# Kernel optimization log

Measured on AMD Instinct MI355X. Metric: run time of the kernel, lower is better.

Reference implementation:

```python
import jax, jax.numpy as jnp
import numpy as np
from jax import lax

B_, NF, H, W = 2, 8, 32, 32
DIM = 384            # mamba_feat_dim = pT*pH*pW*hid_dim = 2*2*2*48
D_INNER = 192        # expand=0.5 -> int(0.5*384)
D_STATE = 16
D_CONV = 4
DT_RANK = 24         # ceil(DIM/16)
HIDDEN = 1536        # mlp_ratio=4
L = NF * H * W


def _ln(x, w, b):
    m = x.mean(-1, keepdims=True)
    v = ((x - m) ** 2).mean(-1, keepdims=True)
    return (x - m) * lax.rsqrt(v + 1e-5) * w + b


def _mamba(xn, in_proj_w, conv_w, conv_b, xproj_w, dt_w, dt_b, A_log, Dp, out_proj_w):
    # xn: [b, L, DIM]
    b = xn.shape[0]
    xz = jnp.einsum('bld,ed->ble', xn, in_proj_w)            # [b,L,2*di]
    xp, z = xz[..., :D_INNER], xz[..., D_INNER:]
    # causal depthwise conv along L (mamba_ssm pads left d_conv-1)
    xc = lax.conv_general_dilated(xp.swapaxes(1, 2), conv_w[:, None, :], (1,),
                                  [(D_CONV - 1, 0)],
                                  dimension_numbers=('NCH', 'OIH', 'NCH'),
                                  feature_group_count=D_INNER) + conv_b[None, :, None]
    xc = jax.nn.silu(xc).swapaxes(1, 2)                      # [b,L,di]
    dbl = jnp.einsum('bld,ed->ble', xc, xproj_w)             # [b,L,dt_rank+2*ds]
    dt = jax.nn.softplus(jnp.einsum('blr,dr->bld', dbl[..., :DT_RANK], dt_w) + dt_b)
    Bm = dbl[..., DT_RANK:DT_RANK + D_STATE]
    Cm = dbl[..., DT_RANK + D_STATE:]
    A = -jnp.exp(A_log)                                      # [di,ds]

    def step(h, inp):
        dt_t, B_t, C_t, x_t = inp                            # [b,di],[b,ds],[b,ds],[b,di]
        dA = jnp.exp(dt_t[..., None] * A)                    # [b,di,ds]
        h = dA * h + dt_t[..., None] * B_t[:, None, :] * x_t[..., None]
        return h, jnp.einsum('bds,bs->bd', h, C_t)

    h0 = jnp.zeros((b, D_INNER, D_STATE), xn.dtype)
    _, ys = lax.scan(step, h0, (dt.swapaxes(0, 1), Bm.swapaxes(0, 1),
                                Cm.swapaxes(0, 1), xc.swapaxes(0, 1)))
    y = ys.swapaxes(0, 1) + Dp * xc
    y = y * jax.nn.silu(z)
    return jnp.einsum('ble,de->bld', y, out_proj_w)


def _ssa(seqs, ssa_w):
    # sequence shuffle attention: grouped 1x1 conv over per-sequence pooled features
    pooled = jnp.stack([s.mean(1) for s in seqs], 1)          # [b,3,c]
    w = jnp.einsum('bsd,dts->btd', pooled, ssa_w)             # per-channel 3x3 mix
    aw = jax.nn.softmax(w, axis=1)                            # softmax over sequences
    st = jnp.stack(seqs, 0)                                   # [3,b,L,c]
    return jnp.einsum('btd,tbld->bld', aw, st)


def _mlp(x, fc1_w, fc1_b, dw_w, dw_b, fc2_w, fc2_b):
    b = x.shape[0]
    h1 = jnp.einsum('bld,ed->ble', x, fc1_w) + fc1_b          # [b,L,HIDDEN]
    hv = h1.swapaxes(1, 2).reshape(b, HIDDEN, NF, H, W)
    hv = lax.conv_general_dilated(hv, dw_w, (1, 1, 1), [(1, 1)] * 3,
                                  dimension_numbers=('NCDHW', 'OIDHW', 'NCDHW'),
                                  feature_group_count=HIDDEN) + dw_b[None, :, None, None, None]
    h1 = hv.reshape(b, HIDDEN, L).swapaxes(1, 2)
    h1 = jax.nn.gelu(h1, approximate=False)
    return jnp.einsum('ble,de->bld', h1, fc2_w) + fc2_b


def _forward(x, freq_x, ln1_w, ln1_b, in_proj_w, conv_w, conv_b, xproj_w, dt_w, dt_b,
             A_log, Dp, out_proj_w, ssa_w, ln2_w, ln2_b, fc1_w, fc1_b, dw_w, dw_b,
             fc2_w, fc2_b, hilbert_curve):
    b = x.shape[0]
    xc = x.transpose(0, 2, 1, 3, 4).reshape(b, DIM, L)        # [b,c,L]
    x_flat = xc[:, :, hilbert_curve].swapaxes(1, 2)           # hilbert gather -> [b,L,c]
    fc = freq_x.transpose(0, 2, 1, 3, 4).reshape(b, DIM, L)
    f_flat = fc[:, :, hilbert_curve].swapaxes(1, 2)
    normed = _ln(x_flat, ln1_w, ln1_b)
    mparams = (in_proj_w, conv_w, conv_b, xproj_w, dt_w, dt_b, A_log, Dp, out_proj_w)
    m_fwd = _mamba(normed, *mparams)
    m_rev = jnp.flip(_mamba(jnp.flip(normed, 1), *mparams), 1)
    mo = _ssa([m_fwd, m_rev, f_flat], ssa_w)
    xm = x_flat + mo
    xm = xm + _mlp(_ln(xm, ln2_w, ln2_b), fc1_w, fc1_b, dw_w, dw_b, fc2_w, fc2_b)
    outm = xm.swapaxes(1, 2)                                  # [b,c,L]
    inv = jnp.argsort(hilbert_curve)                          # inverse permutation (scatter)
    uns = outm[:, :, inv]
    return uns.reshape(b, DIM, NF, H, W).transpose(0, 2, 1, 3, 4)


def setup_inputs() -> dict:
    key = jax.random.key(0)
    ks = jax.random.split(key, 12)
    def n(i, shape, s=0.02):
        return jax.random.normal(ks[i], shape, jnp.float32) * s
    perm = jnp.asarray(np.random.default_rng(0).permutation(L), jnp.int32)
    return {
        'x': jax.random.normal(ks[0], (B_, NF, DIM, H, W), jnp.float32),
        'freq_x': jax.random.normal(ks[1], (B_, NF, DIM, H, W), jnp.float32),
        'hilbert_curve': perm,
        'ln1_w': jnp.ones((DIM,), jnp.float32), 'ln1_b': jnp.zeros((DIM,), jnp.float32),
        'in_proj_w': n(2, (2 * D_INNER, DIM)),
        'conv_w': n(3, (D_INNER, D_CONV), 0.1), 'conv_b': jnp.zeros((D_INNER,), jnp.float32),
        'xproj_w': n(4, (DT_RANK + 2 * D_STATE, D_INNER)),
        'dt_w': n(5, (D_INNER, DT_RANK), 0.1),
        'dt_b': jnp.full((D_INNER,), -4.6, jnp.float32),
        'A_log': jnp.log(jnp.tile(jnp.arange(1, D_STATE + 1, dtype=jnp.float32)[None, :], (D_INNER, 1))),
        'Dp': jnp.ones((D_INNER,), jnp.float32),
        'out_proj_w': n(6, (DIM, D_INNER)),
        'ssa_w': n(7, (DIM, 3, 3)),
        'ln2_w': jnp.ones((DIM,), jnp.float32), 'ln2_b': jnp.zeros((DIM,), jnp.float32),
        'fc1_w': n(8, (HIDDEN, DIM)), 'fc1_b': jnp.zeros((HIDDEN,), jnp.float32),
        'dw_w': n(9, (HIDDEN, 1, 3, 3, 3), 0.05), 'dw_b': jnp.zeros((HIDDEN,), jnp.float32),
        'fc2_w': n(10, (DIM, HIDDEN)), 'fc2_b': jnp.zeros((DIM,), jnp.float32),
    }


def reference(x, freq_x, hilbert_curve, ln1_w, ln1_b, in_proj_w, conv_w, conv_b,
              xproj_w, dt_w, dt_b, A_log, Dp, out_proj_w, ssa_w, ln2_w, ln2_b,
              fc1_w, fc1_b, dw_w, dw_b, fc2_w, fc2_b):
    return _forward(x, freq_x, ln1_w, ln1_b, in_proj_w, conv_w, conv_b, xproj_w,
                    dt_w, dt_b, A_log, Dp, out_proj_w, ssa_w, ln2_w, ln2_b,
                    fc1_w, fc1_b, dw_w, dw_b, fc2_w, fc2_b, hilbert_curve)
```

## Files before the change

### kernel.cpp

```cpp
#include <hip/hip_runtime.h>
#include <cmath>

#define B_N 2
#define NFR 8
#define HH 32
#define WW 32
#define LSEQ 8192
#define DIMD 384
#define DI 192
#define DST 16
#define DRK 24
#define HID 1536
#define MR (B_N*LSEQ)

#define NCH 256
#define CL  (LSEQ/NCH)
#define PSL 128

typedef __attribute__((ext_vector_type(8))) short  bf16x8;
typedef __attribute__((ext_vector_type(4))) float  f32x4;
typedef __attribute__((ext_vector_type(8))) unsigned short u16x8;

constexpr size_t SZ_BLD = (size_t)MR * DIMD;
constexpr size_t SZ_BLI = (size_t)MR * DI;
constexpr size_t SZ_DBL = (size_t)MR * 56;

constexpr size_t OFF_XFLAT = 0;
constexpr size_t OFF_FFLAT = OFF_XFLAT + SZ_BLD;
constexpr size_t OFF_XZ    = OFF_FFLAT + SZ_BLD;
constexpr size_t OFF_XCF   = OFF_XZ + SZ_BLD;
constexpr size_t OFF_XCR   = OFF_XCF + SZ_BLI;
constexpr size_t OFF_H1    = 0;
constexpr size_t OFF_R2    = OFF_XCR + SZ_BLI;
constexpr size_t OFF_DBLF  = OFF_R2;
constexpr size_t OFF_DBLR  = OFF_DBLF + SZ_DBL;
constexpr size_t OFF_DTF   = OFF_DBLR + SZ_DBL;
constexpr size_t OFF_DTR   = OFF_DTF + SZ_BLI;
constexpr size_t OFF_GF    = OFF_DTR + SZ_BLI;
constexpr size_t OFF_GR    = OFF_GF + SZ_BLI;
constexpr size_t OFF_MF    = OFF_GR + SZ_BLI;
constexpr size_t OFF_MR_   = OFF_MF + SZ_BLD;
constexpr size_t OFF_H2    = OFF_R2;
constexpr size_t OFF_NORM  = OFF_MR_ + SZ_BLD;
constexpr size_t OFF_XM    = OFF_NORM + SZ_BLD;
constexpr size_t OFF_PART  = OFF_XM + SZ_BLD;
constexpr size_t OFF_AW    = OFF_PART + (size_t)6*PSL*384;
constexpr size_t OFF_INV   = OFF_AW + 2*3*384;
constexpr size_t SZ_CH   = (size_t)2*B_N*NCH*DI*16;
constexpr size_t OFF_CA  = OFF_NORM;
constexpr size_t OFF_CB  = OFF_CA + SZ_CH;
constexpr size_t OFF_CHS = OFF_CB + SZ_CH;
static_assert(OFF_CHS + SZ_CH <= OFF_PART, "scan summaries overflow");

__device__ __forceinline__ float siluf(float x){ return x / (1.f + expf(-x)); }
__device__ __forceinline__ float softplusf(float x){ return x > 20.f ? x : log1pf(expf(x)); }
__device__ __forceinline__ float geluf(float x){ return 0.5f * x * (1.f + erff(x * 0.70710678118f)); }
__device__ __forceinline__ unsigned short f2bf(float f){
    union { float f; unsigned int u; } v; v.f = f;
    unsigned int u = v.u + 0x7fffu + ((v.u >> 16) & 1u);
    return (unsigned short)(u >> 16);
}

#if __has_builtin(__builtin_amdgcn_global_load_lds)
#define HAVE_GLL 1
__device__ __forceinline__ void gload16(const void* g, void* l){
    __builtin_amdgcn_global_load_lds((const __attribute__((address_space(1))) void*)g,
                                     (__attribute__((address_space(3))) void*)l, 16, 0, 0);
}
#else
#define HAVE_GLL 0
#endif

__global__ __launch_bounds__(256)
void k_inv(const int* __restrict__ hc, int* __restrict__ inv)
{
    int l = blockIdx.x*256 + threadIdx.x;
    inv[hc[l]] = l;
}

__global__ __launch_bounds__(256)
void k_gather_ln(const float* __restrict__ x, const float* __restrict__ fx,
                 const int* __restrict__ inv, const float* __restrict__ lw,
                 const float* __restrict__ lb, float* __restrict__ x_flat,
                 float* __restrict__ f_flat, unsigned short* __restrict__ normed)
{
    __shared__ float tile[DIMD*33];
    int hw0 = blockIdx.x * 32;
    int nf  = blockIdx.y;
    int b   = blockIdx.z;
    int t   = threadIdx.x;
    int hwi = t & 31, dr = t >> 5;
    int w = t >> 6, lane = t & 63;
    const float* xb = x  + ((size_t)(b*NFR+nf)*DIMD)*1024 + hw0;
    const float* fb = fx + ((size_t)(b*NFR+nf)*DIMD)*1024 + hw0;

    for (int d0 = 0; d0 < DIMD; d0 += 8){
        int d = d0 + dr;
        tile[d*33 + hwi] = xb[(size_t)d*1024 + hwi];
    }
    __syncthreads();
    #pragma unroll
    for (int i = 0; i < 8; ++i){
        int r = w*8 + i;
        int l = inv[nf*1024 + hw0 + r];
        size_t rowo = (size_t)(b*LSEQ + l)*DIMD;
        float v[6]; float s = 0.f, s2 = 0.f;
        #pragma unroll
        for (int c = 0; c < 6; ++c){
            float a = tile[(c*64 + lane)*33 + r];
            v[c] = a; s += a; s2 += a*a;
        }
        #pragma unroll
        for (int o = 1; o < 64; o <<= 1){ s += __shfl_xor(s, o); s2 += __shfl_xor(s2, o); }
        float mean = s * (1.f/DIMD);
        float var  = s2 * (1.f/DIMD) - mean*mean;
        float rs = rsqrtf(var + 1e-5f);
        #pragma unroll
        for (int c = 0; c < 6; ++c){
            int d = c*64 + lane;
            x_flat[rowo + d] = v[c];
            normed[rowo + d] = f2bf((v[c]-mean)*rs*lw[d] + lb[d]);
        }
    }
    __syncthreads();
    for (int d0 = 0; d0 < DIMD; d0 += 8){
        int d = d0 + dr;
        tile[d*33 + hwi] = fb[(size_t)d*1024 + hwi];
    }
    __syncthreads();
    #pragma unroll
    for (int i = 0; i < 8; ++i){
        int r = w*8 + i;
        int l = inv[nf*1024 + hw0 + r];
        size_t rowo = (size_t)(b*LSEQ + l)*DIMD;
        #pragma unroll
        for (int c = 0; c < 6; ++c)
            f_flat[rowo + c*64 + lane] = tile[(c*64 + lane)*33 + r];
    }
}

__global__ __launch_bounds__(256)
void k_scatter(const float* __restrict__ outm, const int* __restrict__ inv,
               float* __restrict__ outp)
{
    __shared__ float tile[DIMD*33];
    int hw0 = blockIdx.x * 32;
    int nf  = blockIdx.y;
    int b   = blockIdx.z;
    int t   = threadIdx.x;
    int hwi = t & 31, dr = t >> 5;
    int w = t >> 6, lane = t & 63;
    #pragma unroll
    for (int i = 0; i < 8; ++i){
        int r = w*8 + i;
        int l = inv[nf*1024 + hw0 + r];
        const float* row = outm + (size_t)(b*LSEQ + l)*DIMD;
        #pragma unroll
        for (int c = 0; c < 6; ++c)
            tile[(c*64 + lane)*33 + r] = row[c*64 + lane];
    }
    __syncthreads();
    float* ob = outp + ((size_t)(b*NFR+nf)*DIMD)*1024 + hw0;
    for (int d0 = 0; d0 < DIMD; d0 += 8){
        int d = d0 + dr;
        ob[(size_t)d*1024 + hwi] = tile[d*33 + hwi];
    }
}

__global__ __launch_bounds__(128)
void k_ln(const float* __restrict__ in, const float* __restrict__ lw,
          const float* __restrict__ lb, unsigned short* __restrict__ out)
{
    size_t row = blockIdx.x;
    int t = threadIdx.x;
    float v[3]; float s = 0.f, s2 = 0.f;
    #pragma unroll
    for (int i = 0; i < 3; ++i){
        int d = t + i*128;
        float a = in[row*DIMD + d];
        v[i] = a; s += a; s2 += a*a;
    }
    #pragma unroll
    for (int o = 32; o > 0; o >>= 1){ s += __shfl_down(s, o); s2 += __shfl_down(s2, o); }
    __shared__ float sh[4];
    if ((t & 63) == 0){ sh[(t>>6)*2] = s; sh[(t>>6)*2+1] = s2; }
    __syncthreads();
    float S = sh[0] + sh[2], S2 = sh[1] + sh[3];
    float mean = S * (1.f/DIMD);
    float var  = S2 * (1.f/DIMD) - mean*mean;
    float r = rsqrtf(var + 1e-5f);
    #pragma unroll
    for (int i = 0; i < 3; ++i){
        int d = t + i*128;
        out[row*DIMD + d] = f2bf((v[i]-mean)*r*lw[d] + lb[d]);
    }
}

template<int EPI>
__global__ __launch_bounds__(256, 2)
void k_bgemm(const unsigned short* __restrict__ A, const float* __restrict__ Wf,
             const float* __restrict__ bias, const float* __restrict__ add,
             float* __restrict__ C, int N, int K)
{
    __shared__ unsigned short As[128*32];
    __shared__ unsigned short Bs[128*48];
    int tid  = threadIdx.x;
    int wid  = tid >> 6, lane = tid & 63;
    int row0 = blockIdx.x * 128, col0 = blockIdx.y * 128;
    int wr = wid >> 1, wc = wid & 1;
    int lr = lane & 15, lg = lane >> 4;

    f32x4 acc[4][4];
    #pragma unroll
    for (int m = 0; m < 4; ++m)
        #pragma unroll
        for (int n = 0; n < 4; ++n) acc[m][n] = (f32x4){0.f,0.f,0.f,0.f};

    int sA0 = wid*2048 + lane*16;
    int rA0 = sA0 >> 6, kA0 = (sA0 & 63) >> 1;
    int sA1 = sA0 + 1024;
    int rA1 = sA1 >> 6, kA1 = (sA1 & 63) >> 1;
    const unsigned short* Ag0 = A + (size_t)(row0 + rA0)*K + kA0;
    const unsigned short* Ag1 = A + (size_t)(row0 + rA1)*K + kA1;
    int bn = tid >> 1, bkp = (tid & 1) * 16;
    const float* Wg = Wf + (size_t)(col0 + bn)*K + bkp;

    const unsigned short* Ab = &As[(wr*64 + lr)*32 + lg*8];
    const unsigned short* Bb = &Bs[(wc*64 + lr)*48 + lg*8];
    unsigned short* Bw = &Bs[bn*48 + bkp];

    for (int k0 = 0; k0 < K; k0 += 32){
        if (k0) __syncthreads();
#if HAVE_GLL
        gload16(Ag0, (char*)As + wid*2048);
        gload16(Ag1, (char*)As + wid*2048 + 1024);
#else
        *(u16x8*)((char*)As + sA0) = *(const u16x8*)Ag0;
        *(u16x8*)((char*)As + sA1) = *(const u16x8*)Ag1;
#endif
        Ag0 += 32; Ag1 += 32;
        {
            float4 f0 = *(const float4*)(Wg+0);
            float4 f1 = *(const float4*)(Wg+4);
            float4 f2 = *(const float4*)(Wg+8);
            float4 f3 = *(const float4*)(Wg+12);
            Wg += 32;
            u16x8 p0, p1;
            p0[0]=f2bf(f0.x); p0[1]=f2bf(f0.y); p0[2]=f2bf(f0.z); p0[3]=f2bf(f0.w);
            p0[4]=f2bf(f1.x); p0[5]=f2bf(f1.y); p0[6]=f2bf(f1.z); p0[7]=f2bf(f1.w);
            p1[0]=f2bf(f2.x); p1[1]=f2bf(f2.y); p1[2]=f2bf(f2.z); p1[3]=f2bf(f2.w);
            p1[4]=f2bf(f3.x); p1[5]=f2bf(f3.y); p1[6]=f2bf(f3.z); p1[7]=f2bf(f3.w);
            *(u16x8*)(Bw)     = p0;
            *(u16x8*)(Bw + 8) = p1;
        }
        __syncthreads();
        bf16x8 af[4], bfr[4];
        #pragma unroll
        for (int m = 0; m < 4; ++m) af[m]  = *(const bf16x8*)(Ab + m*512);
        #pragma unroll
        for (int n = 0; n < 4; ++n) bfr[n] = *(const bf16x8*)(Bb + n*768);
        #pragma unroll
        for (int m = 0; m < 4; ++m)
            #pragma unroll
            for (int n = 0; n < 4; ++n)
                acc[m][n] = __builtin_amdgcn_mfma_f32_16x16x32_bf16(af[m], bfr[n], acc[m][n], 0, 0, 0);
    }

    #pragma unroll
    for (int m = 0; m < 4; ++m){
        #pragma unroll
        for (int r = 0; r < 4; ++r){
            int row = row0 + wr*64 + m*16 + lg*4 + r;
            #pragma unroll
            for (int n = 0; n < 4; ++n){
                int col = col0 + wc*64 + n*16 + lr;
                float v = acc[m][n][r];
                if (EPI >= 1) v += bias[col];
                if (EPI == 2) v += add[(size_t)row*N + col];
                C[(size_t)row*N + col] = v;
            }
        }
    }
}

__global__ __launch_bounds__(256)
void k_conv(const float* __restrict__ xz, const float* __restrict__ cw,
            const float* __restrict__ cb, float* __restrict__ xcf, float* __restrict__ xcr)
{
    const int TL = 64;
    int b = blockIdx.y;
    int l0 = blockIdx.x * TL;
    __shared__ float sx[TL+6][DI];
    for (int idx = threadIdx.x; idx < (TL+6)*DI; idx += 256){
        int r = idx / DI, c = idx % DI;
        int l = l0 + r - 3;
        float v = 0.f;
        if (l >= 0 && l < LSEQ) v = xz[((size_t)b*LSEQ + l)*DIMD + c];
        sx[r][c] = v;
    }
    __syncthreads();
    for (int idx = threadIdx.x; idx < TL*DI; idx += 256){
        int r = idx / DI, c = idx % DI;
        float w0 = cw[c*4+0], w1 = cw[c*4+1], w2 = cw[c*4+2], w3 = cw[c*4+3];
        float bi = cb[c];
        size_t orow = ((size_t)b*LSEQ + l0 + r)*DI + c;
        float af = bi + sx[r][c]*w0 + sx[r+1][c]*w1 + sx[r+2][c]*w2 + sx[r+3][c]*w3;
        xcf[orow] = siluf(af);
        float ar = bi + sx[r+3][c]*w3 + sx[r+4][c]*w2 + sx[r+5][c]*w1 + sx[r+6][c]*w0;
        xcr[orow] = siluf(ar);
    }
}

__global__ __launch_bounds__(256)
void k_dbl(const float* __restrict__ xc_f, const float* __restrict__ xc_r,
           const float* __restrict__ xpw,
           float* __restrict__ dbl_f, float* __restrict__ dbl_r)
{
    const float* xc  = blockIdx.y ? xc_r  : xc_f;
    float*       dbl = blockIdx.y ? dbl_r : dbl_f;
    __shared__ float sw[56*196];
    for (int i = threadIdx.x; i < 56*DI; i += 256){
        int n = i / DI, k = i % DI;
        sw[n*196 + k] = xpw[i];
    }
    __syncthreads();
    int lane = threadIdx.x & 63;
    int wid  = threadIdx.x >> 6;
    if (lane >= 56) return;
    const float* wrow = &sw[lane*196];
    #pragma unroll
    for (int g = 0; g < 2; ++g){
        int row0 = blockIdx.x*64 + g*32 + wid*8;
        const float* xr = xc + (size_t)row0*DI;
        float acc[8];
        #pragma unroll
        for (int r = 0; r < 8; ++r) acc[r] = 0.f;
        for (int k = 0; k < DI; k += 4){
            float4 w4 = *(const float4*)&wrow[k];
            #pragma unroll
            for (int r = 0; r < 8; ++r){
                float4 x4 = *(const float4*)&xr[(size_t)r*DI + k];
                acc[r] += x4.x*w4.x + x4.y*w4.y + x4.z*w4.z + x4.w*w4.w;
            }
        }
        #pragma unroll
        for (int r = 0; r < 8; ++r)
            dbl[(size_t)(row0 + r)*56 + lane] = acc[r];
    }
}

__global__ __launch_bounds__(192)
void k_dt(const float* __restrict__ dbl_f, const float* __restrict__ dbl_r,
          const float* __restrict__ dtw, const float* __restrict__ dtb,
          float* __restrict__ dt_f, float* __restrict__ dt_r)
{
    const float* dbl = blockIdx.y ? dbl_r : dbl_f;
    float*       dt  = blockIdx.y ? dt_r  : dt_f;
    int row0 = blockIdx.x * 8;
    int d = threadIdx.x;
    __shared__ float sd[8][24];
    {
        int lr = threadIdx.x / 24, lc = threadIdx.x % 24;
        sd[lr][lc] = dbl[(size_t)(row0 + lr)*56 + lc];
    }
    __syncthreads();
    float wreg[24];
    #pragma unroll
    for (int r = 0; r < DRK; ++r) wreg[r] = dtw[d*DRK + r];
    float bias = dtb[d];
    #pragma unroll
    for (int rr = 0; rr < 8; ++rr){
        float acc = bias;
        #pragma unroll
        for (int r = 0; r < DRK; ++r) acc += sd[rr][r] * wreg[r];
        dt[(size_t)(row0 + rr)*DI + d] = softplusf(acc);
    }
}

__global__ __launch_bounds__(384)
void k_scan_p1(const float* __restrict__ dt_f, const float* __restrict__ dt_r,
               const float* __restrict__ dbl_f, const float* __restrict__ dbl_r,
               const float* __restrict__ xc_f, const float* __restrict__ xc_r,
               const float* __restrict__ A_log,
               float* __restrict__ CA, float* __restrict__ CB)
{
    int ch = blockIdx.x, b = blockIdx.y, dir = blockIdx.z;
    const float* dt  = dir ? dt_r  : dt_f;
    const float* dbl = dir ? dbl_r : dbl_f;
    const float* xc  = dir ? xc_r  : xc_f;
    int t = threadIdx.x;
    int d = t >> 1, sh = (t & 1) * 8;
    float A2[8];
    #pragma unroll
    for (int s = 0; s < 8; ++s) A2[s] = -expf(A_log[d*DST + sh + s]) * 1.44269504f;
    float hB[8];
    #pragma unroll
    for (int s = 0; s < 8; ++s) hB[s] = 0.f;
    float sumdt = 0.f;
    __shared__ float sB[16][16];
    for (int t0 = 0; t0 < CL/16; ++t0){
        __syncthreads();
        if (t < 256){
            int j = t >> 4, c = t & 15;
            int lidx = ch*CL + t0*16 + j;
            int lld = dir ? (LSEQ-1-lidx) : lidx;
            sB[j][c] = dbl[((size_t)b*LSEQ + lld)*56 + 24 + c];
        }
        __syncthreads();
        for (int j = 0; j < 16; ++j){
            int lidx = ch*CL + t0*16 + j;
            int lld = dir ? (LSEQ-1-lidx) : lidx;
            size_t rowbl = (size_t)b*LSEQ + lld;
            float dtv = dt[rowbl*DI + d];
            float xv  = xc[rowbl*DI + d];
            float c0 = dtv * xv;
            sumdt += dtv;
            #pragma unroll
            for (int s = 0; s < 8; ++s){
                float da = exp2f(dtv * A2[s]);
                hB[s] = da*hB[s] + c0*sB[j][sh + s];
            }
        }
    }
    size_t o = (((size_t)(dir*B_N + b)*NCH + ch)*DI + d)*16 + sh;
    #pragma unroll
    for (int s = 0; s < 8; ++s){
        CA[o + s] = exp2f(sumdt * A2[s]);
        CB[o + s] = hB[s];
    }
}

__global__ __launch_bounds__(256)
void k_scan_p2(const float* __restrict__ CA, const float* __restrict__ CB,
               float* __restrict__ CH)
{
    int b = blockIdx.y, dir = blockIdx.z;
    int t = blockIdx.x*256 + threadIdx.x;
    size_t base = ((size_t)(dir*B_N + b)*NCH)*(DI*16) + t;
    float h = 0.f;
    for (int c = 0; c < NCH; ++c){
        size_t o = base + (size_t)c*(DI*16);
        CH[o] = h;
        h = CA[o]*h + CB[o];
    }
}

__global__ __launch_bounds__(384)
void k_scan_p3(const float* __restrict__ dt_f, const float* __restrict__ dt_r,
               const float* __restrict__ dbl_f, const float* __restrict__ dbl_r,
               const float* __restrict__ xc_f, const float* __restrict__ xc_r,
               const float* __restrict__ xz, const float* __restrict__ A_log,
               const float* __restrict__ Dp, const float* __restrict__ CH,
               unsigned short* __restrict__ g_f, unsigned short* __restrict__ g_r)
{
    int ch = blockIdx.x, b = blockIdx.y, dir = blockIdx.z;
    const float* dt  = dir ? dt_r  : dt_f;
    const float* dbl = dir ? dbl_r : dbl_f;
    const float* xc  = dir ? xc_r  : xc_f;
    unsigned short* g = dir ? g_r : g_f;
    int t = threadIdx.x;
    int d = t >> 1, sh = (t & 1) * 8;
    float A2[8];
    #pragma unroll
    for (int s = 0; s < 8; ++s) A2[s] = -expf(A_log[d*DST + sh + s]) * 1.44269504f;
    float Dpd = Dp[d];
    float h[8];
    size_t so = (((size_t)(dir*B_N + b)*NCH + ch)*DI + d)*16 + sh;
    #pragma unroll
    for (int s = 0; s < 8; ++s) h[s] = CH[so + s];
    __shared__ float sBC[16][32];
    for (int t0 = 0; t0 < CL/16; ++t0){
        __syncthreads();
        for (int idx = t; idx < 512; idx += 384){
            int j = idx >> 5, c = idx & 31;
            int lidx = ch*CL + t0*16 + j;
            int lld = dir ? (LSEQ-1-lidx) : lidx;
            sBC[j][c] = dbl[((size_t)b*LSEQ + lld)*56 + 24 + c];
        }
        __syncthreads();
        for (int j = 0; j < 16; ++j){
            int lidx = ch*CL + t0*16 + j;
            int lld = dir ? (LSEQ-1-lidx) : lidx;
            size_t rowbl = (size_t)b*LSEQ + lld;
            float dtv = dt[rowbl*DI + d];
            float xv  = xc[rowbl*DI + d];
            float zv  = xz[rowbl*DIMD + DI + d];
            float c0 = dtv * xv;
            float y = 0.f;
            #pragma unroll
            for (int s = 0; s < 8; ++s){
                float da = exp2f(dtv * A2[s]);
                h[s] = da*h[s] + c0*sBC[j][sh + s];
                y += h[s]*sBC[j][16 + sh + s];
            }
            y += __shfl_xor(y, 1);
            if ((t & 1) == 0)
                g[rowbl*DI + d] = f2bf((y + Dpd*xv) * siluf(zv));
        }
    }
}

__global__ __launch_bounds__(384)
void k_pool(const float* __restrict__ m_f, const float* __restrict__ m_r,
            const float* __restrict__ f_flat, float* __restrict__ partial)
{
    int bt = blockIdx.x;
    int sl = blockIdx.y;
    int b = bt / 3, t = bt % 3;
    const float* src = (t == 0) ? m_f : (t == 1) ? m_r : f_flat;
    src += (size_t)b*LSEQ*DIMD + (size_t)sl*(LSEQ/PSL)*DIMD;
    int d = threadIdx.x;
    float sum = 0.f;
    #pragma unroll 8
    for (int l = 0; l < LSEQ/PSL; ++l) sum += src[(size_t)l*DIMD + d];
    partial[((size_t)bt*PSL + sl)*DIMD + d] = sum;
}

__global__ __launch_bounds__(384)
void k_ssa(const float* __restrict__ partial, const float* __restrict__ ssaw,
           float* __restrict__ aw)
{
    int b = blockIdx.x;
    int d = threadIdx.x;
    float pooled[3];
    #pragma unroll
    for (int t = 0; t < 3; ++t){
        float sum = 0.f;
        for (int sl = 0; sl < PSL; ++sl) sum += partial[((size_t)(b*3+t)*PSL + sl)*DIMD + d];
        pooled[t] = sum * (1.f/LSEQ);
    }
    float wv[3];
    #pragma unroll
    for (int t = 0; t < 3; ++t)
        wv[t] = pooled[0]*ssaw[d*9 + t*3 + 0] + pooled[1]*ssaw[d*9 + t*3 + 1] + pooled[2]*ssaw[d*9 + t*3 + 2];
    float mx = fmaxf(wv[0], fmaxf(wv[1], wv[2]));
    float e0 = expf(wv[0]-mx), e1 = expf(wv[1]-mx), e2 = expf(wv[2]-mx);
    float inv_ = 1.f / (e0+e1+e2);
    aw[(size_t)(b*3+0)*DIMD + d] = e0*inv_;
    aw[(size_t)(b*3+1)*DIMD + d] = e1*inv_;
    aw[(size_t)(b*3+2)*DIMD + d] = e2*inv_;
}

__global__ __launch_bounds__(256)
void k_xm(const float* __restrict__ x_flat, const float* __restrict__ m_f,
          const float* __restrict__ m_r, const float* __restrict__ f_flat,
          const float* __restrict__ aw, float* __restrict__ xm)
{
    size_t idx = (size_t)blockIdx.x*256 + threadIdx.x;
    int d = (int)(idx % DIMD);
    size_t row = idx / DIMD;
    int b = (int)(row >> 13);
    float a0 = aw[(size_t)(b*3+0)*DIMD + d];
    float a1 = aw[(size_t)(b*3+1)*DIMD + d];
    float a2 = aw[(size_t)(b*3+2)*DIMD + d];
    xm[idx] = x_flat[idx] + a0*m_f[idx] + a1*m_r[idx] + a2*f_flat[idx];
}

__global__ __launch_bounds__(256)
void k_dwconv(const float* __restrict__ h1, const float* __restrict__ dww,
              const float* __restrict__ dwb, unsigned short* __restrict__ h2)
{
    int c = blockIdx.x*256 + threadIdx.x;
    int hy = blockIdx.y;
    int h = hy >> 1, w0 = (hy & 1) * 16;
    int bnf = blockIdx.z; int b = bnf >> 3, nf = bnf & 7;
    float wt[27];
    #pragma unroll
    for (int i = 0; i < 27; ++i) wt[i] = dww[(size_t)c*27 + i];
    float bias = dwb[c];
    bool nfok[3], hok[3];
    #pragma unroll
    for (int dd = 0; dd < 3; ++dd){
        nfok[dd] = (nf+dd-1) >= 0 && (nf+dd-1) < NFR;
        hok[dd]  = (h+dd-1)  >= 0 && (h+dd-1)  < HH;
    }
    const float* base = h1 + (size_t)b*LSEQ*HID + c;
    float win[3][3][3];
    #pragma unroll
    for (int dn = 0; dn < 3; ++dn)
        #pragma unroll
        for (int dh = 0; dh < 3; ++dh){
            bool ok = nfok[dn] && hok[dh];
            size_t rb = ((size_t)(nf+dn-1)*1024 + (size_t)(h+dh-1)*32);
            win[dn][dh][0] = (ok && w0 > 0) ? base[(rb + w0-1)*HID] : 0.f;
            win[dn][dh][1] = ok ? base[(rb + w0  )*HID] : 0.f;
            win[dn][dh][2] = ok ? base[(rb + w0+1)*HID] : 0.f;
        }
    unsigned short* orow = h2 + ((size_t)b*LSEQ + nf*1024 + h*32)*HID + c;
    #pragma unroll
    for (int xw = 0; xw < 16; ++xw){
        float acc = bias;
        #pragma unroll
        for (int dn = 0; dn < 3; ++dn)
            #pragma unroll
            for (int dh = 0; dh < 3; ++dh)
                #pragma unroll
                for (int dw = 0; dw < 3; ++dw)
                    acc += win[dn][dh][dw] * wt[dn*9 + dh*3 + dw];
        orow[(size_t)(w0 + xw)*HID] = f2bf(geluf(acc));
        int wn = w0 + xw + 2;
        #pragma unroll
        for (int dn = 0; dn < 3; ++dn)
            #pragma unroll
            for (int dh = 0; dh < 3; ++dh){
                win[dn][dh][0] = win[dn][dh][1];
                win[dn][dh][1] = win[dn][dh][2];
                bool ok = (wn < WW) && nfok[dn] && hok[dh];
                size_t rb = ((size_t)(nf+dn-1)*1024 + (size_t)(h+dh-1)*32);
                win[dn][dh][2] = ok ? base[(rb + wn)*HID] : 0.f;
            }
    }
}

extern "C" void kernel_launch(void* const* d_in, const int* in_sizes, int n_in,
                              void* d_out, int out_size, void* d_ws, size_t ws_size,
                              hipStream_t stream)
{
    const float* x     = (const float*)d_in[0];
    const float* fx    = (const float*)d_in[1];
    const int*   hc    = (const int*)  d_in[2];
    const float* ln1w  = (const float*)d_in[3];
    const float* ln1b  = (const float*)d_in[4];
    const float* inpw  = (const float*)d_in[5];
    const float* convw = (const float*)d_in[6];
    const float* convb = (const float*)d_in[7];
    const float* xpw   = (const float*)d_in[8];
    const float* dtw   = (const float*)d_in[9];
    const float* dtb   = (const float*)d_in[10];
    const float* alog  = (const float*)d_in[11];
    const float* dp    = (const float*)d_in[12];
    const float* outpw = (const float*)d_in[13];
    const float* ssaw  = (const float*)d_in[14];
    const float* ln2w  = (const float*)d_in[15];
    const float* ln2b  = (const float*)d_in[16];
    const float* fc1w  = (const float*)d_in[17];
    const float* fc1b  = (const float*)d_in[18];
    const float* dww   = (const float*)d_in[19];
    const float* dwb   = (const float*)d_in[20];
    const float* fc2w  = (const float*)d_in[21];
    const float* fc2b  = (const float*)d_in[22];

    float* ws = (float*)d_ws;
    float* x_flat = ws + OFF_XFLAT;
    float* f_flat = ws + OFF_FFLAT;
    float* xz     = ws + OFF_XZ;
    float* xc_f   = ws + OFF_XCF;
    float* xc_r   = ws + OFF_XCR;
    float* dbl_f  = ws + OFF_DBLF;
    float* dbl_r  = ws + OFF_DBLR;
    float* dt_f   = ws + OFF_DTF;
    float* dt_r   = ws + OFF_DTR;
    float* m_f    = ws + OFF_MF;
    float* m_r    = ws + OFF_MR_;
    float* h1     = ws + OFF_H1;
    float* xm     = ws + OFF_XM;
    float* part   = ws + OFF_PART;
    float* aw     = ws + OFF_AW;
    float* cA     = ws + OFF_CA;
    float* cB     = ws + OFF_CB;
    float* cH     = ws + OFF_CHS;
    float* outm   = ws + OFF_NORM;
    int*   inv    = (int*)(ws + OFF_INV);
    unsigned short* nrm_bf = (unsigned short*)(ws + OFF_NORM);
    unsigned short* gf_bf  = (unsigned short*)(ws + OFF_GF);
    unsigned short* gr_bf  = (unsigned short*)(ws + OFF_GR);
    unsigned short* h2_bf  = (unsigned short*)(ws + OFF_H2);
    float* outp   = (float*)d_out;

    k_inv<<<LSEQ/256, 256, 0, stream>>>(hc, inv);
    k_gather_ln<<<dim3(32, NFR, B_N), 256, 0, stream>>>(x, fx, inv, ln1w, ln1b, x_flat, f_flat, nrm_bf);
    k_bgemm<0><<<dim3(128,3), 256, 0, stream>>>(nrm_bf, inpw, nullptr, nullptr, xz, DIMD, DIMD);
    k_conv<<<dim3(LSEQ/64, B_N), 256, 0, stream>>>(xz, convw, convb, xc_f, xc_r);
    k_dbl<<<dim3(MR/64, 2), 256, 0, stream>>>(xc_f, xc_r, xpw, dbl_f, dbl_r);
    k_dt<<<dim3(MR/8, 2), 192, 0, stream>>>(dbl_f, dbl_r, dtw, dtb, dt_f, dt_r);
    k_scan_p1<<<dim3(NCH, B_N, 2), 384, 0, stream>>>(dt_f, dt_r, dbl_f, dbl_r, xc_f, xc_r, alog, cA, cB);
    k_scan_p2<<<dim3(DI*16/256, B_N, 2), 256, 0, stream>>>(cA, cB, cH);
    k_scan_p3<<<dim3(NCH, B_N, 2), 384, 0, stream>>>(dt_f, dt_r, dbl_f, dbl_r, xc_f, xc_r, xz, alog, dp, cH, gf_bf, gr_bf);
    k_bgemm<0><<<dim3(128,3), 256, 0, stream>>>(gf_bf, outpw, nullptr, nullptr, m_f, DIMD, DI);
    k_bgemm<0><<<dim3(128,3), 256, 0, stream>>>(gr_bf, outpw, nullptr, nullptr, m_r, DIMD, DI);
    k_pool<<<dim3(6,PSL), 384, 0, stream>>>(m_f, m_r, f_flat, part);
    k_ssa<<<B_N, 384, 0, stream>>>(part, ssaw, aw);
    k_xm<<<(unsigned)(SZ_BLD/256), 256, 0, stream>>>(x_flat, m_f, m_r, f_flat, aw, xm);
    k_ln<<<MR, 128, 0, stream>>>(xm, ln2w, ln2b, nrm_bf);
    k_bgemm<1><<<dim3(128,12), 256, 0, stream>>>(nrm_bf, fc1w, fc1b, nullptr, h1, HID, DIMD);
    k_dwconv<<<dim3(6,64,16), 256, 0, stream>>>(h1, dww, dwb, h2_bf);
    k_bgemm<2><<<dim3(128,3), 256, 0, stream>>>(h2_bf, fc2w, fc2b, xm, outm, DIMD, HID);
    k_scatter<<<dim3(32, NFR, B_N), 256, 0, stream>>>(outm, inv, outp);
}
```

Baseline: 620.5 us.

## Split-K the fc2 GEMM and stage scan inputs through shared memory

The fc2 GEMM is split into two K halves across a third grid dimension. The second partial goes to a scratch buffer and is added during the final scatter, raising the block count for a long-K GEMM. Both scan passes now load dt, xc and z tiles with coalesced float4 loads into LDS instead of per-thread scattered global reads. The output pointer is also stepped incrementally. This adds an extra full-size partial buffer write and read, plus more LDS use per block.

```diff
diff --git a/kernel.cpp b/kernel.cpp
--- a/kernel.cpp
+++ b/kernel.cpp
@@ -31,6 +31,7 @@
 constexpr size_t OFF_XCF   = OFF_XZ + SZ_BLD;
 constexpr size_t OFF_XCR   = OFF_XCF + SZ_BLI;
 constexpr size_t OFF_H1    = 0;
+constexpr size_t OFF_P1    = 0;
 constexpr size_t OFF_R2    = OFF_XCR + SZ_BLI;
 constexpr size_t OFF_DBLF  = OFF_R2;
 constexpr size_t OFF_DBLR  = OFF_DBLF + SZ_DBL;
@@ -140,8 +141,8 @@
 }
 
 __global__ __launch_bounds__(256)
-void k_scatter(const float* __restrict__ outm, const int* __restrict__ inv,
-               float* __restrict__ outp)
+void k_scatter(const float* __restrict__ outm, const float* __restrict__ p1,
+               const int* __restrict__ inv, float* __restrict__ outp)
 {
     __shared__ float tile[DIMD*33];
     int hw0 = blockIdx.x * 32;
@@ -154,10 +155,12 @@
     for (int i = 0; i < 8; ++i){
         int r = w*8 + i;
         int l = inv[nf*1024 + hw0 + r];
-        const float* row = outm + (size_t)(b*LSEQ + l)*DIMD;
+        size_t rowo = (size_t)(b*LSEQ + l)*DIMD;
+        const float* row = outm + rowo;
+        const float* prw = p1 + rowo;
         #pragma unroll
         for (int c = 0; c < 6; ++c)
-            tile[(c*64 + lane)*33 + r] = row[c*64 + lane];
+            tile[(c*64 + lane)*33 + r] = row[c*64 + lane] + prw[c*64 + lane];
     }
     __syncthreads();
     float* ob = outp + ((size_t)(b*NFR+nf)*DIMD)*1024 + hw0;
@@ -200,7 +203,7 @@
 __global__ __launch_bounds__(256, 2)
 void k_bgemm(const unsigned short* __restrict__ A, const float* __restrict__ Wf,
              const float* __restrict__ bias, const float* __restrict__ add,
-             float* __restrict__ C, int N, int K)
+             float* __restrict__ C, int N, int Kext, int Kstr)
 {
     __shared__ unsigned short As[128*32];
     __shared__ unsigned short Bs[128*48];
@@ -220,16 +223,16 @@
     int rA0 = sA0 >> 6, kA0 = (sA0 & 63) >> 1;
     int sA1 = sA0 + 1024;
     int rA1 = sA1 >> 6, kA1 = (sA1 & 63) >> 1;
-    const unsigned short* Ag0 = A + (size_t)(row0 + rA0)*K + kA0;
-    const unsigned short* Ag1 = A + (size_t)(row0 + rA1)*K + kA1;
+    const unsigned short* Ag0 = A + (size_t)(row0 + rA0)*Kstr + kA0;
+    const unsigned short* Ag1 = A + (size_t)(row0 + rA1)*Kstr + kA1;
     int bn = tid >> 1, bkp = (tid & 1) * 16;
-    const float* Wg = Wf + (size_t)(col0 + bn)*K + bkp;
+    const float* Wg = Wf + (size_t)(col0 + bn)*Kstr + bkp;
 
     const unsigned short* Ab = &As[(wr*64 + lr)*32 + lg*8];
     const unsigned short* Bb = &Bs[(wc*64 + lr)*48 + lg*8];
     unsigned short* Bw = &Bs[bn*48 + bkp];
 
-    for (int k0 = 0; k0 < K; k0 += 32){
+    for (int k0 = 0; k0 < Kext; k0 += 32){
         if (k0) __syncthreads();
 #if HAVE_GLL
         gload16(Ag0, (char*)As + wid*2048);
@@ -283,6 +286,97 @@
     }
 }
 
+__global__ __launch_bounds__(256, 2)
+void k_bgemm_sk(const unsigned short* __restrict__ A, const float* __restrict__ Wf,
+                const float* __restrict__ bias, const float* __restrict__ add,
+                float* __restrict__ C0, float* __restrict__ C1, int N, int Khalf, int Kstr)
+{
+    __shared__ unsigned short As[128*32];
+    __shared__ unsigned short Bs[128*48];
+    int tid  = threadIdx.x;
+    int wid  = tid >> 6, lane = tid & 63;
+    int row0 = blockIdx.x * 128, col0 = blockIdx.y * 128;
+    int z = blockIdx.z;
+    int kbeg = z * Khalf;
+    int wr = wid >> 1, wc = wid & 1;
+    int lr = lane & 15, lg = lane >> 4;
+
+    f32x4 acc[4][4];
+    #pragma unroll
+    for (int m = 0; m < 4; ++m)
+        #pragma unroll
+        for (int n = 0; n < 4; ++n) acc[m][n] = (f32x4){0.f,0.f,0.f,0.f};
+
+    int sA0 = wid*2048 + lane*16;
+    int rA0 = sA0 >> 6, kA0 = (sA0 & 63) >> 1;
+    int sA1 = sA0 + 1024;
+    int rA1 = sA1 >> 6, kA1 = (sA1 & 63) >> 1;
+    const unsigned short* Ag0 = A + (size_t)(row0 + rA0)*Kstr + kbeg + kA0;
+    const unsigned short* Ag1 = A + (size_t)(row0 + rA1)*Kstr + kbeg + kA1;
+    int bn = tid >> 1, bkp = (tid & 1) * 16;
+    const float* Wg = Wf + (size_t)(col0 + bn)*Kstr + kbeg + bkp;
+
+    const unsigned short* Ab = &As[(wr*64 + lr)*32 + lg*8];
+    const unsigned short* Bb = &Bs[(wc*64 + lr)*48 + lg*8];
+    unsigned short* Bw = &Bs[bn*48 + bkp];
+
+    for (int k0 = 0; k0 < Khalf; k0 += 32){
+        if (k0) __syncthreads();
+#if HAVE_GLL
+        gload16(Ag0, (char*)As + wid*2048);
+        gload16(Ag1, (char*)As + wid*2048 + 1024);
+#else
+        *(u16x8*)((char*)As + sA0) = *(const u16x8*)Ag0;
+        *(u16x8*)((char*)As + sA1) = *(const u16x8*)Ag1;
+#endif
+        Ag0 += 32; Ag1 += 32;
+        {
+            float4 f0 = *(const float4*)(Wg+0);
+            float4 f1 = *(const float4*)(Wg+4);
+            float4 f2 = *(const float4*)(Wg+8);
+            float4 f3 = *(const float4*)(Wg+12);
+            Wg += 32;
+            u16x8 p0, p1;
+            p0[0]=f2bf(f0.x); p0[1]=f2bf(f0.y); p0[2]=f2bf(f0.z); p0[3]=f2bf(f0.w);
+            p0[4]=f2bf(f1.x); p0[5]=f2bf(f1.y); p0[6]=f2bf(f1.z); p0[7]=f2bf(f1.w);
+            p1[0]=f2bf(f2.x); p1[1]=f2bf(f2.y); p1[2]=f2bf(f2.z); p1[3]=f2bf(f2.w);
+            p1[4]=f2bf(f3.x); p1[5]=f2bf(f3.y); p1[6]=f2bf(f3.z); p1[7]=f2bf(f3.w);
+            *(u16x8*)(Bw)     = p0;
+            *(u16x8*)(Bw + 8) = p1;
+        }
+        __syncthreads();
+        bf16x8 af[4], bfr[4];
+        #pragma unroll
+        for (int m = 0; m < 4; ++m) af[m]  = *(const bf16x8*)(Ab + m*512);
+        #pragma unroll
+        for (int n = 0; n < 4; ++n) bfr[n] = *(const bf16x8*)(Bb + n*768);
+        #pragma unroll
+        for (int m = 0; m < 4; ++m)
+            #pragma unroll
+            for (int n = 0; n < 4; ++n)
+                acc[m][n] = __builtin_amdgcn_mfma_f32_16x16x32_bf16(af[m], bfr[n], acc[m][n], 0, 0, 0);
+    }
+
+    #pragma unroll
+    for (int m = 0; m < 4; ++m){
+        #pragma unroll
+        for (int r = 0; r < 4; ++r){
+            int row = row0 + wr*64 + m*16 + lg*4 + r;
+            #pragma unroll
+            for (int n = 0; n < 4; ++n){
+                int col = col0 + wc*64 + n*16 + lr;
+                float v = acc[m][n][r];
+                if (z == 0){
+                    v += bias[col] + add[(size_t)row*N + col];
+                    C0[(size_t)row*N + col] = v;
+                } else {
+                    C1[(size_t)row*N + col] = v;
+                }
+            }
+        }
+    }
+}
+
 __global__ __launch_bounds__(256)
 void k_conv(const float* __restrict__ xz, const float* __restrict__ cw,
             const float* __restrict__ cb, float* __restrict__ xcf, float* __restrict__ xcr)
@@ -397,9 +491,19 @@
     #pragma unroll
     for (int s = 0; s < 8; ++s) hB[s] = 0.f;
     float sumdt = 0.f;
-    __shared__ float sB[16][16];
+    __shared__ float sdt[16][192], sxc[16][192], sB[16][16];
     for (int t0 = 0; t0 < CL/16; ++t0){
         __syncthreads();
+        #pragma unroll
+        for (int q = 0; q < 2; ++q){
+            int idx = t + q*384;
+            int j = idx / 48, c4 = (idx % 48)*4;
+            int lidx = ch*CL + t0*16 + j;
+            int lld = dir ? (LSEQ-1-lidx) : lidx;
+            size_t rowbl = (size_t)b*LSEQ + lld;
+            *(float4*)&sdt[j][c4] = *(const float4*)&dt[rowbl*DI + c4];
+            *(float4*)&sxc[j][c4] = *(const float4*)&xc[rowbl*DI + c4];
+        }
         if (t < 256){
             int j = t >> 4, c = t & 15;
             int lidx = ch*CL + t0*16 + j;
@@ -407,13 +511,10 @@
             sB[j][c] = dbl[((size_t)b*LSEQ + lld)*56 + 24 + c];
         }
         __syncthreads();
+        #pragma unroll 4
         for (int j = 0; j < 16; ++j){
-            int lidx = ch*CL + t0*16 + j;
-            int lld = dir ? (LSEQ-1-lidx) : lidx;
-            size_t rowbl = (size_t)b*LSEQ + lld;
-            float dtv = dt[rowbl*DI + d];
-            float xv  = xc[rowbl*DI + d];
-            float c0 = dtv * xv;
+            float dtv = sdt[j][d];
+            float c0  = dtv * sxc[j][d];
             sumdt += dtv;
             #pragma unroll
             for (int s = 0; s < 8; ++s){
@@ -468,9 +569,23 @@
     size_t so = (((size_t)(dir*B_N + b)*NCH + ch)*DI + d)*16 + sh;
     #pragma unroll
     for (int s = 0; s < 8; ++s) h[s] = CH[so + s];
-    __shared__ float sBC[16][32];
+    __shared__ float sdt[16][192], sxc[16][192], szv[16][192], sBC[16][32];
+    int lld0 = dir ? (LSEQ-1 - ch*CL) : (ch*CL);
+    long gstep = dir ? -(long)DI : (long)DI;
+    unsigned short* gp = g + ((size_t)b*LSEQ + lld0)*DI + d;
     for (int t0 = 0; t0 < CL/16; ++t0){
         __syncthreads();
+        #pragma unroll
+        for (int q = 0; q < 2; ++q){
+            int idx = t + q*384;
+            int j = idx / 48, c4 = (idx % 48)*4;
+            int lidx = ch*CL + t0*16 + j;
+            int lld = dir ? (LSEQ-1-lidx) : lidx;
+            size_t rowbl = (size_t)b*LSEQ + lld;
+            *(float4*)&sdt[j][c4] = *(const float4*)&dt[rowbl*DI + c4];
+            *(float4*)&sxc[j][c4] = *(const float4*)&xc[rowbl*DI + c4];
+            *(float4*)&szv[j][c4] = *(const float4*)&xz[rowbl*DIMD + DI + c4];
+        }
         for (int idx = t; idx < 512; idx += 384){
             int j = idx >> 5, c = idx & 31;
             int lidx = ch*CL + t0*16 + j;
@@ -478,14 +593,11 @@
             sBC[j][c] = dbl[((size_t)b*LSEQ + lld)*56 + 24 + c];
         }
         __syncthreads();
+        #pragma unroll 4
         for (int j = 0; j < 16; ++j){
-            int lidx = ch*CL + t0*16 + j;
-            int lld = dir ? (LSEQ-1-lidx) : lidx;
-            size_t rowbl = (size_t)b*LSEQ + lld;
-            float dtv = dt[rowbl*DI + d];
-            float xv  = xc[rowbl*DI + d];
-            float zv  = xz[rowbl*DIMD + DI + d];
-            float c0 = dtv * xv;
+            float dtv = sdt[j][d];
+            float xv  = sxc[j][d];
+            float c0  = dtv * xv;
             float y = 0.f;
             #pragma unroll
             for (int s = 0; s < 8; ++s){
@@ -494,8 +606,11 @@
                 y += h[s]*sBC[j][16 + sh + s];
             }
             y += __shfl_xor(y, 1);
-            if ((t & 1) == 0)
-                g[rowbl*DI + d] = f2bf((y + Dpd*xv) * siluf(zv));
+            if ((t & 1) == 0){
+                float zv = szv[j][d];
+                *gp = f2bf((y + Dpd*xv) * siluf(zv));
+            }
+            gp += gstep;
         }
     }
 }
@@ -653,6 +768,7 @@
     float* m_f    = ws + OFF_MF;
     float* m_r    = ws + OFF_MR_;
     float* h1     = ws + OFF_H1;
+    float* p1buf  = ws + OFF_P1;
     float* xm     = ws + OFF_XM;
     float* part   = ws + OFF_PART;
     float* aw     = ws + OFF_AW;
@@ -669,21 +785,21 @@
 
     k_inv<<<LSEQ/256, 256, 0, stream>>>(hc, inv);
     k_gather_ln<<<dim3(32, NFR, B_N), 256, 0, stream>>>(x, fx, inv, ln1w, ln1b, x_flat, f_flat, nrm_bf);
-    k_bgemm<0><<<dim3(128,3), 256, 0, stream>>>(nrm_bf, inpw, nullptr, nullptr, xz, DIMD, DIMD);
+    k_bgemm<0><<<dim3(128,3), 256, 0, stream>>>(nrm_bf, inpw, nullptr, nullptr, xz, DIMD, DIMD, DIMD);
     k_conv<<<dim3(LSEQ/64, B_N), 256, 0, stream>>>(xz, convw, convb, xc_f, xc_r);
     k_dbl<<<dim3(MR/64, 2), 256, 0, stream>>>(xc_f, xc_r, xpw, dbl_f, dbl_r);
     k_dt<<<dim3(MR/8, 2), 192, 0, stream>>>(dbl_f, dbl_r, dtw, dtb, dt_f, dt_r);
     k_scan_p1<<<dim3(NCH, B_N, 2), 384, 0, stream>>>(dt_f, dt_r, dbl_f, dbl_r, xc_f, xc_r, alog, cA, cB);
     k_scan_p2<<<dim3(DI*16/256, B_N, 2), 256, 0, stream>>>(cA, cB, cH);
     k_scan_p3<<<dim3(NCH, B_N, 2), 384, 0, stream>>>(dt_f, dt_r, dbl_f, dbl_r, xc_f, xc_r, xz, alog, dp, cH, gf_bf, gr_bf);
-    k_bgemm<0><<<dim3(128,3), 256, 0, stream>>>(gf_bf, outpw, nullptr, nullptr, m_f, DIMD, DI);
-    k_bgemm<0><<<dim3(128,3), 256, 0, stream>>>(gr_bf, outpw, nullptr, nullptr, m_r, DIMD, DI);
+    k_bgemm<0><<<dim3(128,3), 256, 0, stream>>>(gf_bf, outpw, nullptr, nullptr, m_f, DIMD, DI, DI);
+    k_bgemm<0><<<dim3(128,3), 256, 0, stream>>>(gr_bf, outpw, nullptr, nullptr, m_r, DIMD, DI, DI);
     k_pool<<<dim3(6,PSL), 384, 0, stream>>>(m_f, m_r, f_flat, part);
     k_ssa<<<B_N, 384, 0, stream>>>(part, ssaw, aw);
     k_xm<<<(unsigned)(SZ_BLD/256), 256, 0, stream>>>(x_flat, m_f, m_r, f_flat, aw, xm);
     k_ln<<<MR, 128, 0, stream>>>(xm, ln2w, ln2b, nrm_bf);
-    k_bgemm<1><<<dim3(128,12), 256, 0, stream>>>(nrm_bf, fc1w, fc1b, nullptr, h1, HID, DIMD);
+    k_bgemm<1><<<dim3(128,12), 256, 0, stream>>>(nrm_bf, fc1w, fc1b, nullptr, h1, HID, DIMD, DIMD);
     k_dwconv<<<dim3(6,64,16), 256, 0, stream>>>(h1, dww, dwb, h2_bf);
-    k_bgemm<2><<<dim3(128,3), 256, 0, stream>>>(h2_bf, fc2w, fc2b, xm, outm, DIMD, HID);
-    k_scatter<<<dim3(32, NFR, B_N), 256, 0, stream>>>(outm, inv, outp);
-}
+    k_bgemm_sk<<<dim3(128,3,2), 256, 0, stream>>>(h2_bf, fc2w, fc2b, xm, outm, p1buf, DIMD, HID/2, HID);
+    k_scatter<<<dim3(32, NFR, B_N), 256, 0, stream>>>(outm, p1buf, inv, outp);
+}
```

New measurement: 604.7 us. 1.03x faster.
